# Kernel tuning notes

Measured on AMD Instinct MI355X. Metric: run time of the kernel, lower is better.

## Reference

```python
import jax, jax.numpy as jnp
import numpy as np

B, N, M, K = 2, 65536, 8192, 32
N_CY = N_CONE = N_DISK = N_ELLIP = 16
TOTAL_GIBS = N_CY + N_CONE + N_DISK + N_ELLIP
NUM_OBSERVERS = 16
KERNEL_REACH = 1.0
EPS = 1e-8


def setup_inputs() -> dict:
    key = jax.random.key(0)
    ks = jax.random.split(key, 10)
    points = jax.random.normal(ks[0], (B, N, 3), dtype=jnp.float32)
    q_coords = jax.random.normal(ks[1], (B, M, 3), dtype=jnp.float32)
    support_idxs = jax.random.randint(ks[2], (B, M, K), 0, N)
    mc_points = jax.random.normal(ks[3], (1024, 3), dtype=jnp.float32)
    # per-GIB geometric params, positive, within kernel reach (random_init analogue)
    u = lambda k, shp: 0.1 + (KERNEL_REACH - 0.1) * jax.random.uniform(k, shp, dtype=jnp.float32)
    cy_params = u(ks[4], (N_CY, 2))      # [radius, sigma]
    cone_params = u(ks[5], (N_CONE, 2))  # [slope, sigma]
    disk_params = u(ks[6], (N_DISK, 2))  # [radius, height]
    ellip_params = u(ks[7], (N_ELLIP, 3))  # [rx, ry, rz]
    # cvx coefficients: softmax over GIB axis (maintain_convexity at init)
    lambdas = jax.nn.softmax(jax.random.normal(ks[8], (TOTAL_GIBS, NUM_OBSERVERS), dtype=jnp.float32), axis=0)
    return {"points": points, "q_coords": q_coords, "support_idxs": support_idxs,
            "mc_points": mc_points, "cy_params": cy_params, "cone_params": cone_params,
            "disk_params": disk_params, "ellip_params": ellip_params, "lambdas": lambdas}


def _gib_outputs(points, q_coords, support_idxs, cy_p, cone_p, disk_p, ellip_p):
    # shared neighborhood gather: (B, M, K, 3)
    supp = points[jnp.arange(points.shape[0])[:, None, None], support_idxs]
    rel = supp - q_coords[:, :, None, :]
    rx, ry, rz = rel[..., 0], rel[..., 1], rel[..., 2]
    r2 = rx * rx + ry * ry                     # (B, M, K) squared radial dist
    r2e, rze = r2[..., None], rz[..., None]    # (B, M, K, 1)
    # cylinder: gaussian shell around radius in the xy-plane
    cy = jnp.exp(-(r2e - cy_p[:, 0] ** 2) ** 2 / (2.0 * cy_p[:, 1] ** 2 + EPS))
    # cone: radial distance tracks slope * height
    cone = jnp.exp(-(jnp.sqrt(r2e + EPS) - cone_p[:, 0] * rze) ** 2 / (2.0 * cone_p[:, 1] ** 2 + EPS))
    # disk: flattened gaussian (wide radially, thin in z)
    disk = jnp.exp(-r2e / (disk_p[:, 0] ** 2 + EPS) - rze ** 2 / (disk_p[:, 1] ** 2 + EPS))
    # ellipsoid: anisotropic gaussian
    el = jnp.exp(-(rx[..., None] ** 2 / (ellip_p[:, 0] ** 2 + EPS)
                   + ry[..., None] ** 2 / (ellip_p[:, 1] ** 2 + EPS)
                   + rz[..., None] ** 2 / (ellip_p[:, 2] ** 2 + EPS)))
    # reduce over neighborhood K, then stack GIBs: (B, M, total_gibs)
    return jnp.concatenate([cy.mean(axis=2), cone.mean(axis=2),
                            disk.mean(axis=2), el.mean(axis=2)], axis=-1)


def reference(points, q_coords, support_idxs, mc_points, cy_params, cone_params,
              disk_params, ellip_params, lambdas):
    q_out = _gib_outputs(points, q_coords, support_idxs,
                         cy_params, cone_params, disk_params, ellip_params)
    # observers: convex combination of GIB responses -> (B, M, num_observers)
    return q_out @ lambdas
```

## Files before the change

kernel.cpp:

```cpp
#include <hip/hip_runtime.h>


#define EPSF 1e-8f
#define LOG2E 1.4426950408889634f

constexpr int LAM_STRIDE = 18;

__global__ __launch_bounds__(256, 8) void gib_kernel(
    const float* __restrict__ points,
    const float* __restrict__ qc,
    const int*   __restrict__ sidx,
    const float* __restrict__ cyp,
    const float* __restrict__ conep,
    const float* __restrict__ diskp,
    const float* __restrict__ ellp,
    const float* __restrict__ lam,
    float*       __restrict__ out)
{
    __shared__ float lamS[64 * LAM_STRIDE];

    const int tid = threadIdx.x;

    {
        int g = tid >> 2, o = (tid & 3) * 4;
#pragma unroll
        for (int j = 0; j < 4; j++)
            lamS[g * LAM_STRIDE + o + j] = lam[g * 16 + o + j] * (1.0f / 32.0f);
    }
    __syncthreads();

    const int l  = tid & 63;
    const int c  = l & 31;
    const int qh = l >> 5;
    const int q  = blockIdx.x * 8 + (tid >> 6) * 2 + qh;
    const int b  = q >> 13;

    float al1, al2, al3, al4, nb0, A1, B1, C1;
    if (c < 16) {
        float c0 = cyp[2 * c], c1 = cyp[2 * c + 1];
        al1 = 1.f; al2 = 0.f; al3 = 0.f; al4 = -c0 * c0;
        nb0 = -LOG2E / (2.f * c1 * c1 + EPSF);
        float d0 = diskp[2 * c], d1 = diskp[2 * c + 1];
        float ai = -LOG2E / (d0 * d0 + EPSF);
        A1 = ai; B1 = ai; C1 = -LOG2E / (d1 * d1 + EPSF);
    } else {
        int cc = c - 16;
        float k0 = conep[2 * cc], k1 = conep[2 * cc + 1];
        al1 = 0.f; al2 = 1.f; al3 = -k0; al4 = 0.f;
        nb0 = -LOG2E / (2.f * k1 * k1 + EPSF);
        float e0 = ellp[3 * cc], e1 = ellp[3 * cc + 1], e2 = ellp[3 * cc + 2];
        A1 = -LOG2E / (e0 * e0 + EPSF);
        B1 = -LOG2E / (e1 * e1 + EPSF);
        C1 = -LOG2E / (e2 * e2 + EPSF);
    }

    const float* qq = qc + q * 3;
    const float qx = qq[0], qy = qq[1], qz = qq[2];
    const float* ptbase = points + (size_t)(b << 16) * 3;
    const int4*  idxp   = (const int4*)(sidx + q * 32);

    float a0 = 0.f, a1 = 0.f;
#pragma unroll
    for (int jc = 0; jc < 8; jc++) {
        const int4 i4 = idxp[jc];
        const int ii[4] = {i4.x, i4.y, i4.z, i4.w};
#pragma unroll
        for (int j = 0; j < 4; j++) {
            const float* pp = ptbase + ii[j] * 3;
            float rx = pp[0] - qx;
            float ry = pp[1] - qy;
            float rz = pp[2] - qz;
            float rx2 = rx * rx, ry2 = ry * ry, rz2 = rz * rz;
            float r2 = rx2 + ry2;
            float s  = __builtin_amdgcn_sqrtf(r2 + EPSF);
            float u  = fmaf(al1, r2, fmaf(al2, s, fmaf(al3, rz, al4)));
            a0 += __builtin_amdgcn_exp2f(u * u * nb0);
            float v  = fmaf(rx2, A1, fmaf(ry2, B1, rz2 * C1));
            a1 += __builtin_amdgcn_exp2f(v);
        }
    }

    float sv[16];
    {
        const float* ra = &lamS[c * LAM_STRIDE];
        const float* rb = &lamS[(32 + c) * LAM_STRIDE];
#define GIB_MV(o, slot) { float2 La = *(const float2*)&ra[o]; float2 Lb = *(const float2*)&rb[o]; \
        sv[slot##0] = fmaf(a0, La.x, a1 * Lb.x); sv[slot##1] = fmaf(a0, La.y, a1 * Lb.y); }
        { float2 La = *(const float2*)&ra[0];  float2 Lb = *(const float2*)&rb[0];
          sv[0]  = fmaf(a0, La.x, a1 * Lb.x); sv[8]  = fmaf(a0, La.y, a1 * Lb.y); }
        { float2 La = *(const float2*)&ra[2];  float2 Lb = *(const float2*)&rb[2];
          sv[4]  = fmaf(a0, La.x, a1 * Lb.x); sv[12] = fmaf(a0, La.y, a1 * Lb.y); }
        { float2 La = *(const float2*)&ra[4];  float2 Lb = *(const float2*)&rb[4];
          sv[2]  = fmaf(a0, La.x, a1 * Lb.x); sv[10] = fmaf(a0, La.y, a1 * Lb.y); }
        { float2 La = *(const float2*)&ra[6];  float2 Lb = *(const float2*)&rb[6];
          sv[6]  = fmaf(a0, La.x, a1 * Lb.x); sv[14] = fmaf(a0, La.y, a1 * Lb.y); }
        { float2 La = *(const float2*)&ra[8];  float2 Lb = *(const float2*)&rb[8];
          sv[1]  = fmaf(a0, La.x, a1 * Lb.x); sv[9]  = fmaf(a0, La.y, a1 * Lb.y); }
        { float2 La = *(const float2*)&ra[10]; float2 Lb = *(const float2*)&rb[10];
          sv[5]  = fmaf(a0, La.x, a1 * Lb.x); sv[13] = fmaf(a0, La.y, a1 * Lb.y); }
        { float2 La = *(const float2*)&ra[12]; float2 Lb = *(const float2*)&rb[12];
          sv[3]  = fmaf(a0, La.x, a1 * Lb.x); sv[11] = fmaf(a0, La.y, a1 * Lb.y); }
        { float2 La = *(const float2*)&ra[14]; float2 Lb = *(const float2*)&rb[14];
          sv[7]  = fmaf(a0, La.x, a1 * Lb.x); sv[15] = fmaf(a0, La.y, a1 * Lb.y); }
#undef GIB_MV
    }

    {
        bool up = (c & 1);
#pragma unroll
        for (int i = 0; i < 8; i++) {
            float keep = up ? sv[i + 8] : sv[i];
            float send = up ? sv[i] : sv[i + 8];
            sv[i] = keep + __shfl_xor(send, 1, 64);
        }
    }
    {
        bool up = (c & 2);
#pragma unroll
        for (int i = 0; i < 4; i++) {
            float keep = up ? sv[i + 4] : sv[i];
            float send = up ? sv[i] : sv[i + 4];
            sv[i] = keep + __shfl_xor(send, 2, 64);
        }
    }
    {
        bool up = (c & 4);
#pragma unroll
        for (int i = 0; i < 2; i++) {
            float keep = up ? sv[i + 2] : sv[i];
            float send = up ? sv[i] : sv[i + 2];
            sv[i] = keep + __shfl_xor(send, 4, 64);
        }
    }
    {
        bool up = (c & 8);
        float keep = up ? sv[1] : sv[0];
        float send = up ? sv[0] : sv[1];
        sv[0] = keep + __shfl_xor(send, 8, 64);
    }
    sv[0] += __shfl_xor(sv[0], 16, 64);

    if (c < 16)
        out[q * 16 + c] = sv[0];
}

extern "C" void kernel_launch(void* const* d_in, const int* in_sizes, int n_in,
                              void* d_out, int out_size, void* d_ws, size_t ws_size,
                              hipStream_t stream) {
    const float* points = (const float*)d_in[0];
    const float* qc     = (const float*)d_in[1];
    const int*   sidx   = (const int*)d_in[2];
    const float* cyp    = (const float*)d_in[4];
    const float* conep  = (const float*)d_in[5];
    const float* diskp  = (const float*)d_in[6];
    const float* ellp   = (const float*)d_in[7];
    const float* lam    = (const float*)d_in[8];
    float*       out    = (float*)d_out;

    const int totalQ = 2 * 8192;
    dim3 grid(totalQ / 8), block(256);
    hipLaunchKernelGGL(gib_kernel, grid, block, 0, stream,
                       points, qc, sidx, cyp, conep, diskp, ellp, lam, out);
}
```

Before: 84.49 us.

## Gather neighbor offsets cooperatively into shared memory before per-GIB evaluation

Each thread now gathers a single neighbor point, computes its offset from the query plus the radial sqrt, and stores them as a float4 in LDS. Previously every one of 32 lanes per query reloaded all 32 indices and points from global memory. The evaluation loop then reads the offsets as LDS broadcasts, which removes redundant global gathers and the repeated sqrt. In exchange it adds 4 KB of shared memory and a barrier placed before the compute loop.

```diff
diff --git a/kernel.cpp b/kernel.cpp
--- a/kernel.cpp
+++ b/kernel.cpp
@@ -17,9 +17,26 @@
     const float* __restrict__ lam,
     float*       __restrict__ out)
 {
-    __shared__ float lamS[64 * LAM_STRIDE];
+    __shared__ float  lamS[64 * LAM_STRIDE];
+    __shared__ float4 relS[256];
 
     const int tid = threadIdx.x;
+
+    {
+        const int ql = tid >> 5;
+        const int kk = tid & 31;
+        const int qg = blockIdx.x * 8 + ql;
+        const int bb = qg >> 13;
+        const int idx = sidx[qg * 32 + kk];
+        const float* pp = points + ((size_t)(bb << 16) + (size_t)idx) * 3;
+        const float* qq = qc + qg * 3;
+        float rx = pp[0] - qq[0];
+        float ry = pp[1] - qq[1];
+        float rz = pp[2] - qq[2];
+        float r2 = rx * rx + ry * ry;
+        float s  = __builtin_amdgcn_sqrtf(r2 + EPSF);
+        relS[tid] = make_float4(rx, ry, rz, s);
+    }
 
     {
         int g = tid >> 2, o = (tid & 3) * 4;
@@ -27,13 +44,10 @@
         for (int j = 0; j < 4; j++)
             lamS[g * LAM_STRIDE + o + j] = lam[g * 16 + o + j] * (1.0f / 32.0f);
     }
-    __syncthreads();
 
     const int l  = tid & 63;
     const int c  = l & 31;
-    const int qh = l >> 5;
-    const int q  = blockIdx.x * 8 + (tid >> 6) * 2 + qh;
-    const int b  = q >> 13;
+    const int q  = blockIdx.x * 8 + (tid >> 5);
 
     float al1, al2, al3, al4, nb0, A1, B1, C1;
     if (c < 16) {
@@ -54,38 +68,26 @@
         C1 = -LOG2E / (e2 * e2 + EPSF);
     }
 
-    const float* qq = qc + q * 3;
-    const float qx = qq[0], qy = qq[1], qz = qq[2];
-    const float* ptbase = points + (size_t)(b << 16) * 3;
-    const int4*  idxp   = (const int4*)(sidx + q * 32);
+    __syncthreads();
+
+    const float4* rel = &relS[(tid >> 5) * 32];
 
     float a0 = 0.f, a1 = 0.f;
 #pragma unroll
-    for (int jc = 0; jc < 8; jc++) {
-        const int4 i4 = idxp[jc];
-        const int ii[4] = {i4.x, i4.y, i4.z, i4.w};
-#pragma unroll
-        for (int j = 0; j < 4; j++) {
-            const float* pp = ptbase + ii[j] * 3;
-            float rx = pp[0] - qx;
-            float ry = pp[1] - qy;
-            float rz = pp[2] - qz;
-            float rx2 = rx * rx, ry2 = ry * ry, rz2 = rz * rz;
-            float r2 = rx2 + ry2;
-            float s  = __builtin_amdgcn_sqrtf(r2 + EPSF);
-            float u  = fmaf(al1, r2, fmaf(al2, s, fmaf(al3, rz, al4)));
-            a0 += __builtin_amdgcn_exp2f(u * u * nb0);
-            float v  = fmaf(rx2, A1, fmaf(ry2, B1, rz2 * C1));
-            a1 += __builtin_amdgcn_exp2f(v);
-        }
+    for (int k = 0; k < 32; k++) {
+        float4 p = rel[k];
+        float rx2 = p.x * p.x, ry2 = p.y * p.y, rz2 = p.z * p.z;
+        float r2 = rx2 + ry2;
+        float u  = fmaf(al1, r2, fmaf(al2, p.w, fmaf(al3, p.z, al4)));
+        a0 += __builtin_amdgcn_exp2f(u * u * nb0);
+        float v  = fmaf(rx2, A1, fmaf(ry2, B1, rz2 * C1));
+        a1 += __builtin_amdgcn_exp2f(v);
     }
 
     float sv[16];
     {
         const float* ra = &lamS[c * LAM_STRIDE];
         const float* rb = &lamS[(32 + c) * LAM_STRIDE];
-#define GIB_MV(o, slot) { float2 La = *(const float2*)&ra[o]; float2 Lb = *(const float2*)&rb[o]; \
-        sv[slot##0] = fmaf(a0, La.x, a1 * Lb.x); sv[slot##1] = fmaf(a0, La.y, a1 * Lb.y); }
         { float2 La = *(const float2*)&ra[0];  float2 Lb = *(const float2*)&rb[0];
           sv[0]  = fmaf(a0, La.x, a1 * Lb.x); sv[8]  = fmaf(a0, La.y, a1 * Lb.y); }
         { float2 La = *(const float2*)&ra[2];  float2 Lb = *(const float2*)&rb[2];
@@ -102,7 +104,6 @@
           sv[3]  = fmaf(a0, La.x, a1 * Lb.x); sv[11] = fmaf(a0, La.y, a1 * Lb.y); }
         { float2 La = *(const float2*)&ra[14]; float2 Lb = *(const float2*)&rb[14];
           sv[7]  = fmaf(a0, La.x, a1 * Lb.x); sv[15] = fmaf(a0, La.y, a1 * Lb.y); }
-#undef GIB_MV
     }
 
     {
```

Result: no change. 84.67 us (+0.2%).
